# Kernel optimization log

Hardware: AMD Instinct MI355X
Metric: run time of the kernel (lower is better)

## Reference

```python
import jax, jax.numpy as jnp
import numpy as np

N_EXPERTS = 8
TOP_K = 2
HIDDEN = 768
INTER = 2048

def setup_inputs() -> dict:
    key = jax.random.key(0)
    ks = jax.random.split(key, 12)
    s_in = 1.0 / np.sqrt(HIDDEN)
    s_mid = 1.0 / np.sqrt(INTER)
    return {
        "x": jax.random.normal(ks[0], (4, 64, 64, HIDDEN), dtype=jnp.float32),
        # gate: nn.Parameter(randn(E, d))
        "gate_w": jax.random.normal(ks[1], (N_EXPERTS, HIDDEN), dtype=jnp.float32),
        # routed experts, stacked: fc1 (d->f), fc2 (f->d)
        "fc1_w": jax.random.uniform(ks[2], (N_EXPERTS, INTER, HIDDEN), jnp.float32, -s_in, s_in),
        "fc1_b": jax.random.uniform(ks[3], (N_EXPERTS, INTER), jnp.float32, -s_in, s_in),
        "fc2_w": jax.random.uniform(ks[4], (N_EXPERTS, HIDDEN, INTER), jnp.float32, -s_mid, s_mid),
        "fc2_b": jax.random.uniform(ks[5], (N_EXPERTS, HIDDEN), jnp.float32, -s_mid, s_mid),
        # shared MLP (gated): w1 (d->f), w3 (d->f), w2 (f->d)
        "w1_w": jax.random.uniform(ks[6], (INTER, HIDDEN), jnp.float32, -s_in, s_in),
        "w1_b": jax.random.uniform(ks[7], (INTER,), jnp.float32, -s_in, s_in),
        "w3_w": jax.random.uniform(ks[8], (INTER, HIDDEN), jnp.float32, -s_in, s_in),
        "w3_b": jax.random.uniform(ks[9], (INTER,), jnp.float32, -s_in, s_in),
        "w2_w": jax.random.uniform(ks[10], (HIDDEN, INTER), jnp.float32, -s_mid, s_mid),
        "w2_b": jax.random.uniform(ks[11], (HIDDEN,), jnp.float32, -s_mid, s_mid),
    }

def _gelu(h):
    # torch nn.GELU / F.gelu default = exact (erf) form
    return jax.nn.gelu(h, approximate=False)

def reference(x, gate_w, fc1_w, fc1_b, fc2_w, fc2_b,
              w1_w, w1_b, w3_w, w3_b, w2_w, w2_b):
    B, H, W, C = x.shape
    xf = x.reshape(-1, C)                                  # [T, d]
    # gate: softmax over experts, top-k, renormalize
    scores = jax.nn.softmax(xf @ gate_w.T, axis=-1)        # [T, E]
    top_v, top_i = jax.lax.top_k(scores, TOP_K)            # [T, k]
    top_v = top_v / jnp.sum(top_v, axis=-1, keepdims=True)
    # routed experts: dense-mask combine (weight 0 => zero contribution,
    # same math as gather-GEMM-scatter without data-dependent shapes)
    out = jnp.zeros_like(xf)
    for e in range(N_EXPERTS):
        w_e = jnp.sum(jnp.where(top_i == e, top_v, 0.0), axis=-1)   # [T]
        h = _gelu(xf @ fc1_w[e].T + fc1_b[e])                        # [T, f]
        y = h @ fc2_w[e].T + fc2_b[e]                                # [T, d]
        out = out + w_e[:, None] * y
    # shared gated MLP
    shared = (_gelu(xf @ w1_w.T + w1_b) * (xf @ w3_w.T + w3_b)) @ w2_w.T + w2_b
    return (out + shared).reshape(B, H, W, C)
```

## Files before the change

### kernel.cpp

```cpp
#include <hip/hip_runtime.h>
#include <math.h>

#define T_TOK 16384
#define DH 768
#define DF 2048
#define NE 8
#define NSLOT (2 * T_TOK)
#define MT_ROUTED 264
#define NROW_H (MT_ROUTED * 128)

typedef __attribute__((ext_vector_type(8))) short bf16x8;
typedef __attribute__((ext_vector_type(4))) float f32x4;

__device__ __forceinline__ unsigned short f2bf(float f) {
  union { float f; unsigned int u; } v; v.f = f;
  unsigned int u = v.u;
  u += 0x7fffu + ((u >> 16) & 1u);
  return (unsigned short)(u >> 16);
}

__device__ __forceinline__ float gelu_exact(float x) {
  return 0.5f * x * (1.0f + erff(x * 0.70710678118654752440f));
}

__device__ __forceinline__ void async_cp16(void* lds, const void* g) {
  __builtin_amdgcn_global_load_lds(
      (const __attribute__((address_space(1))) unsigned int*)(unsigned long long)g,
      (__attribute__((address_space(3))) unsigned int*)(unsigned int)(unsigned long long)lds,
      16, 0, 0);
}

__global__ __launch_bounds__(256) void conv_f32_bf16(
    const float* __restrict__ src, unsigned short* __restrict__ dst, int n4) {
  int i = blockIdx.x * blockDim.x + threadIdx.x;
  if (i >= n4) return;
  const float4 v = ((const float4*)src)[i];
  union { unsigned short us[4]; unsigned long long u64; } o;
  o.us[0] = f2bf(v.x); o.us[1] = f2bf(v.y); o.us[2] = f2bf(v.z); o.us[3] = f2bf(v.w);
  ((unsigned long long*)dst)[i] = o.u64;
}

__global__ __launch_bounds__(256) void gate_topk(
    const float* __restrict__ x, const float* __restrict__ gw,
    unsigned short* __restrict__ xb, int* __restrict__ eids,
    float* __restrict__ wts) {
  const int wave = threadIdx.x >> 6;
  const int lane = threadIdx.x & 63;
  const int t = blockIdx.x * 4 + wave;
  float4 xv[3];
#pragma unroll
  for (int i = 0; i < 3; ++i) {
    const int c = i * 256 + lane * 4;
    xv[i] = *(const float4*)&x[(long)t * DH + c];
    ushort4 o;
    o.x = f2bf(xv[i].x); o.y = f2bf(xv[i].y);
    o.z = f2bf(xv[i].z); o.w = f2bf(xv[i].w);
    *(ushort4*)&xb[(long)t * DH + c] = o;
  }
  float s[NE];
#pragma unroll
  for (int e = 0; e < NE; ++e) {
    float a = 0.f;
#pragma unroll
    for (int i = 0; i < 3; ++i) {
      const float4 g = *(const float4*)&gw[e * DH + i * 256 + lane * 4];
      a += xv[i].x * g.x + xv[i].y * g.y + xv[i].z * g.z + xv[i].w * g.w;
    }
    s[e] = a;
  }
#pragma unroll
  for (int off = 32; off >= 1; off >>= 1) {
#pragma unroll
    for (int e = 0; e < NE; ++e) s[e] += __shfl_xor(s[e], off);
  }
  if (lane == 0) {
    float b1 = s[0]; int i1 = 0;
#pragma unroll
    for (int e = 1; e < NE; ++e) { if (s[e] > b1) { b1 = s[e]; i1 = e; } }
    float b2 = -3.4e38f; int i2 = 0;
#pragma unroll
    for (int e = 0; e < NE; ++e) {
      if (e != i1 && s[e] > b2) { b2 = s[e]; i2 = e; }
    }
    const float ex = expf(b2 - b1);
    eids[2 * t]     = i1; wts[2 * t]     = 1.f / (1.f + ex);
    eids[2 * t + 1] = i2; wts[2 * t + 1] = ex / (1.f + ex);
  }
}

__global__ __launch_bounds__(256) void hist_k(
    const int* __restrict__ eids, int* __restrict__ hcur) {
  const int j = blockIdx.x * 256 + threadIdx.x;
  const int lane = threadIdx.x & 63;
  const int eid = eids[j];
#pragma unroll
  for (int e = 0; e < NE; ++e) {
    const unsigned long long m = __ballot(eid == e);
    const int tot = __popcll(m);
    if (tot && lane == (__ffsll((long long)m) - 1)) atomicAdd(&hcur[e * 64], tot);
  }
}

__global__ void scan_k(const int* __restrict__ hcur, int* __restrict__ sched,
                       int* __restrict__ cur2) {
  if (threadIdx.x == 0) {
    int b = 0;
#pragma unroll
    for (int e = 0; e < NE; ++e) {
      const int c = hcur[e * 64];
      sched[e] = b; sched[9 + e] = c; cur2[e * 64] = b;
      b += (c + 127) & ~127;
    }
    sched[8] = b;
  }
}

__global__ __launch_bounds__(256) void scatter_k(
    const int* __restrict__ eids, const float* __restrict__ wts,
    int* __restrict__ cur2, int* __restrict__ slot_tok,
    float* __restrict__ slot_wt) {
  const int j = blockIdx.x * 256 + threadIdx.x;
  const int lane = threadIdx.x & 63;
  const int eid = eids[j];
  const float w = wts[j];
#pragma unroll
  for (int e = 0; e < NE; ++e) {
    const unsigned long long m = __ballot(eid == e);
    const int tot = __popcll(m);
    if (!tot) continue;
    const int leader = __ffsll((long long)m) - 1;
    int b = 0;
    if (lane == leader) b = atomicAdd(&cur2[e * 64], tot);
    b = __shfl(b, leader);
    if (eid == e) {
      const int pos = b + __popcll(m & ((1ull << lane) - 1));
      slot_tok[pos] = j;
      slot_wt[pos] = w;
    }
  }
}

template <int MODE>
__global__ __launch_bounds__(256, 2) void gemm_k(
    const unsigned short* __restrict__ A, const unsigned short* __restrict__ B1,
    const unsigned short* __restrict__ B2, const float* __restrict__ bias1,
    const float* __restrict__ bias2, float* __restrict__ outF,
    unsigned short* __restrict__ outH, int K,
    const int* __restrict__ sched, const int* __restrict__ slot_tok,
    const float* __restrict__ slot_wt) {
  const int tid = threadIdx.x;
  const int wave = tid >> 6;
  const int lane = tid & 63;
  const int wm = wave >> 1, wn = wave & 1;
  const int l16 = lane & 15, quad = lane >> 4;
  const int n0 = blockIdx.x * 128;
  const int m0 = blockIdx.y * 128;

  const unsigned short* Bbase = B1;
  const float* bias = bias1;
  int cnt_end = 0;
  if constexpr (MODE == 1 || MODE == 3) {
    if (m0 >= sched[8]) return;
    int e = 0;
#pragma unroll
    for (int i = 1; i < NE; ++i) { if (m0 >= sched[i]) e = i; }
    cnt_end = sched[e] + sched[9 + e];
    Bbase = B1 + (long)e * ((MODE == 1) ? (long)DF * DH : (long)DH * DF);
    bias = bias1 + e * ((MODE == 1) ? DF : DH);
  }

  __shared__ __align__(16) unsigned short As[128 * 32];
  __shared__ __align__(16) unsigned short Bs[128 * 32];
  __shared__ __align__(16) unsigned short Cs[(MODE == 0) ? 128 * 32 : 16];

  const int srow0 = wave * 16 + (lane >> 2);
  const int srow1 = 64 + srow0;
  const int scol = (lane & 3) * 8;

  long ar0, ar1;
  if constexpr (MODE == 1) {
    const int p0 = m0 + srow0, p1 = m0 + srow1;
    const int t0 = (p0 < cnt_end) ? (slot_tok[p0] >> 1) : 0;
    const int t1 = (p1 < cnt_end) ? (slot_tok[p1] >> 1) : 0;
    ar0 = (long)t0 * K; ar1 = (long)t1 * K;
  } else {
    ar0 = (long)(m0 + srow0) * K;
    ar1 = (long)(m0 + srow1) * K;
  }
  const unsigned short* ap0 = A + ar0 + scol;
  const unsigned short* ap1 = A + ar1 + scol;
  const unsigned short* bp0 = Bbase + (long)(n0 + srow0) * K + scol;
  const unsigned short* bp1 = Bbase + (long)(n0 + srow1) * K + scol;
  const unsigned short* cp0 = nullptr; const unsigned short* cp1 = nullptr;
  if constexpr (MODE == 0) {
    cp0 = B2 + (long)(n0 + srow0) * K + scol;
    cp1 = B2 + (long)(n0 + srow1) * K + scol;
  }

  unsigned short* AsW = &As[wave * 512];
  unsigned short* BsW = &Bs[wave * 512];
  unsigned short* CsW = nullptr;
  if constexpr (MODE == 0) CsW = &Cs[wave * 512];

  f32x4 acc[4][4];
  f32x4 acc2[(MODE == 0) ? 4 : 1][(MODE == 0) ? 4 : 1];
#pragma unroll
  for (int i = 0; i < 4; ++i) {
#pragma unroll
    for (int j = 0; j < 4; ++j) {
      acc[i][j] = {0.f, 0.f, 0.f, 0.f};
      if constexpr (MODE == 0) acc2[i][j] = {0.f, 0.f, 0.f, 0.f};
    }
  }

  const int KT = K >> 5;
  for (int kt = 0; kt < KT; ++kt) {
    const int ko = kt << 5;
    async_cp16(AsW,        ap0 + ko);
    async_cp16(AsW + 2048, ap1 + ko);
    async_cp16(BsW,        bp0 + ko);
    async_cp16(BsW + 2048, bp1 + ko);
    if constexpr (MODE == 0) {
      async_cp16(CsW,        cp0 + ko);
      async_cp16(CsW + 2048, cp1 + ko);
    }
    __syncthreads();

    bf16x8 af[4], bfr[4], cfr[(MODE == 0) ? 4 : 1];
#pragma unroll
    for (int mi = 0; mi < 4; ++mi)
      af[mi] = *(const bf16x8*)&As[(wm * 64 + mi * 16 + l16) * 32 + quad * 8];
#pragma unroll
    for (int ni = 0; ni < 4; ++ni) {
      bfr[ni] = *(const bf16x8*)&Bs[(wn * 64 + ni * 16 + l16) * 32 + quad * 8];
      if constexpr (MODE == 0)
        cfr[ni] = *(const bf16x8*)&Cs[(wn * 64 + ni * 16 + l16) * 32 + quad * 8];
    }
#pragma unroll
    for (int mi = 0; mi < 4; ++mi) {
#pragma unroll
      for (int ni = 0; ni < 4; ++ni) {
        acc[mi][ni] = __builtin_amdgcn_mfma_f32_16x16x32_bf16(
            af[mi], bfr[ni], acc[mi][ni], 0, 0, 0);
        if constexpr (MODE == 0)
          acc2[mi][ni] = __builtin_amdgcn_mfma_f32_16x16x32_bf16(
              af[mi], cfr[ni], acc2[mi][ni], 0, 0, 0);
      }
    }
    __syncthreads();
  }

#pragma unroll
  for (int mi = 0; mi < 4; ++mi) {
#pragma unroll
    for (int r = 0; r < 4; ++r) {
      const int row = m0 + wm * 64 + mi * 16 + quad * 4 + r;
      if constexpr (MODE == 3) {
        if (row < cnt_end) {
          const int t = slot_tok[row] >> 1;
          const float w = slot_wt[row];
#pragma unroll
          for (int ni = 0; ni < 4; ++ni) {
            const int c = n0 + wn * 64 + ni * 16 + l16;
            atomicAdd(&outF[(long)t * DH + c], w * (acc[mi][ni][r] + bias[c]));
          }
        }
      } else if constexpr (MODE == 2) {
#pragma unroll
        for (int ni = 0; ni < 4; ++ni) {
          const int c = n0 + wn * 64 + ni * 16 + l16;
          outF[(long)row * DH + c] = acc[mi][ni][r] + bias[c];
        }
      } else if constexpr (MODE == 1) {
#pragma unroll
        for (int ni = 0; ni < 4; ++ni) {
          const int c = n0 + wn * 64 + ni * 16 + l16;
          outH[(long)row * DF + c] = f2bf(gelu_exact(acc[mi][ni][r] + bias[c]));
        }
      } else {
#pragma unroll
        for (int ni = 0; ni < 4; ++ni) {
          const int c = n0 + wn * 64 + ni * 16 + l16;
          const float h1 = acc[mi][ni][r] + bias[c];
          const float h3 = acc2[mi][ni][r] + bias2[c];
          outH[(long)row * DF + c] = f2bf(gelu_exact(h1) * h3);
        }
      }
    }
  }
}

extern "C" void kernel_launch(void* const* d_in, const int* in_sizes, int n_in,
                              void* d_out, int out_size, void* d_ws, size_t ws_size,
                              hipStream_t stream) {
  const float* x     = (const float*)d_in[0];
  const float* gw    = (const float*)d_in[1];
  const float* fc1w  = (const float*)d_in[2];
  const float* fc1bs = (const float*)d_in[3];
  const float* fc2w  = (const float*)d_in[4];
  const float* fc2bs = (const float*)d_in[5];
  const float* w1w   = (const float*)d_in[6];
  const float* w1bs  = (const float*)d_in[7];
  const float* w3w   = (const float*)d_in[8];
  const float* w3bs  = (const float*)d_in[9];
  const float* w2w   = (const float*)d_in[10];
  const float* w2bs  = (const float*)d_in[11];
  float* out = (float*)d_out;

  char* p = (char*)d_ws;
  auto take = [&](size_t b) { char* r = p; p += (b + 255) & ~(size_t)255; return r; };
  unsigned short* xb   = (unsigned short*)take((size_t)T_TOK * DH * 2);
  unsigned short* fc1b = (unsigned short*)take((size_t)NE * DF * DH * 2);
  unsigned short* fc2b = (unsigned short*)take((size_t)NE * DH * DF * 2);
  unsigned short* w1b  = (unsigned short*)take((size_t)DF * DH * 2);
  unsigned short* w3b  = (unsigned short*)take((size_t)DF * DH * 2);
  unsigned short* w2b  = (unsigned short*)take((size_t)DH * DF * 2);
  unsigned short* h    = (unsigned short*)take((size_t)NROW_H * DF * 2);
  int*   eids     = (int*)take((size_t)NSLOT * 4);
  float* wts      = (float*)take((size_t)NSLOT * 4);
  int*   hcur     = (int*)take(NE * 64 * 4);
  int*   cur2     = (int*)take(NE * 64 * 4);
  int*   sched    = (int*)take(32 * 4);
  int*   slot_tok = (int*)take((size_t)NROW_H * 4);
  float* slot_wt  = (float*)take((size_t)NROW_H * 4);

  hipMemsetAsync(hcur, 0, NE * 64 * sizeof(int), stream);

  auto conv = [&](const float* s, unsigned short* d, long n) {
    int n4 = (int)(n >> 2);
    conv_f32_bf16<<<(n4 + 255) / 256, 256, 0, stream>>>(s, d, n4);
  };
  conv(fc1w, fc1b, (long)NE * DF * DH);
  conv(fc2w, fc2b, (long)NE * DH * DF);
  conv(w1w, w1b, (long)DF * DH);
  conv(w3w, w3b, (long)DF * DH);
  conv(w2w, w2b, (long)DH * DF);

  gate_topk<<<T_TOK / 4, 256, 0, stream>>>(x, gw, xb, eids, wts);
  hist_k<<<NSLOT / 256, 256, 0, stream>>>(eids, hcur);
  scan_k<<<1, 64, 0, stream>>>(hcur, sched, cur2);
  scatter_k<<<NSLOT / 256, 256, 0, stream>>>(eids, wts, cur2, slot_tok, slot_wt);

  gemm_k<0><<<dim3(DF / 128, T_TOK / 128), 256, 0, stream>>>(
      xb, w1b, w3b, w1bs, w3bs, nullptr, h, DH, nullptr, nullptr, nullptr);
  gemm_k<2><<<dim3(DH / 128, T_TOK / 128), 256, 0, stream>>>(
      h, w2b, nullptr, w2bs, nullptr, out, nullptr, DF, nullptr, nullptr, nullptr);

  gemm_k<1><<<dim3(DF / 128, MT_ROUTED), 256, 0, stream>>>(
      xb, fc1b, nullptr, fc1bs, nullptr, nullptr, h, DH, sched, slot_tok, slot_wt);
  gemm_k<3><<<dim3(DH / 128, MT_ROUTED), 256, 0, stream>>>(
      h, fc2b, nullptr, fc2bs, nullptr, out, nullptr, DF, sched, slot_tok, slot_wt);
}
```

Baseline: 851.1 us.

## Replace routed atomic scatter with bf16 staging combined in shared-MLP epilogue

The routed fc2 GEMM no longer scatters with float atomicAdd into the output. It writes per-slot results as bf16 rows into a staging buffer that reuses the converted fc1 weight region plus an extra workspace chunk. The shared w2 GEMM epilogue then gathers each token's two slot rows through a new slot_pos map and adds the weighted expert outputs, so every output element is written once. GEMM launches also become 1D grids with an XCD-interleaved block-to-tile mapping. The cost is an extra bf16 round-trip and rounding of the expert outputs, and the old atomic path is kept as a fallback when the workspace is too small.

```diff
diff --git a/kernel.cpp b/kernel.cpp
--- a/kernel.cpp
+++ b/kernel.cpp
@@ -18,9 +18,17 @@
   u += 0x7fffu + ((u >> 16) & 1u);
   return (unsigned short)(u >> 16);
 }
+__device__ __forceinline__ float bf2f(unsigned short s) {
+  union { unsigned int u; float f; } v; v.u = ((unsigned int)s) << 16; return v.f;
+}
 
 __device__ __forceinline__ float gelu_exact(float x) {
   return 0.5f * x * (1.0f + erff(x * 0.70710678118654752440f));
+}
+
+__device__ __forceinline__ unsigned short* yrow(unsigned short* ylo,
+                                                unsigned short* yhi, int s) {
+  return (s < T_TOK) ? (ylo + (long)s * DH) : (yhi + (long)(s - T_TOK) * DH);
 }
 
 __device__ __forceinline__ void async_cp16(void* lds, const void* g) {
@@ -118,7 +126,7 @@
 __global__ __launch_bounds__(256) void scatter_k(
     const int* __restrict__ eids, const float* __restrict__ wts,
     int* __restrict__ cur2, int* __restrict__ slot_tok,
-    float* __restrict__ slot_wt) {
+    float* __restrict__ slot_wt, int* __restrict__ slot_pos) {
   const int j = blockIdx.x * 256 + threadIdx.x;
   const int lane = threadIdx.x & 63;
   const int eid = eids[j];
@@ -136,36 +144,42 @@
       const int pos = b + __popcll(m & ((1ull << lane) - 1));
       slot_tok[pos] = j;
       slot_wt[pos] = w;
-    }
-  }
-}
-
-template <int MODE>
+      slot_pos[j] = pos;
+    }
+  }
+}
+
+template <int MODE, int GX, int GTOT>
 __global__ __launch_bounds__(256, 2) void gemm_k(
     const unsigned short* __restrict__ A, const unsigned short* __restrict__ B1,
     const unsigned short* __restrict__ B2, const float* __restrict__ bias1,
     const float* __restrict__ bias2, float* __restrict__ outF,
     unsigned short* __restrict__ outH, int K,
     const int* __restrict__ sched, const int* __restrict__ slot_tok,
-    const float* __restrict__ slot_wt) {
+    const int* __restrict__ slot_pos, const float* __restrict__ wts,
+    unsigned short* __restrict__ ylo, unsigned short* __restrict__ yhi) {
+  constexpr int BPX = (GTOT + 7) / 8;
+  const int id = blockIdx.x;
+  const int yx = (id & 7) * BPX + (id >> 3);
+  const int n0 = (yx % GX) * 128;
+  const int m0 = (yx / GX) * 128;
+
   const int tid = threadIdx.x;
   const int wave = tid >> 6;
   const int lane = tid & 63;
   const int wm = wave >> 1, wn = wave & 1;
   const int l16 = lane & 15, quad = lane >> 4;
-  const int n0 = blockIdx.x * 128;
-  const int m0 = blockIdx.y * 128;
 
   const unsigned short* Bbase = B1;
   const float* bias = bias1;
   int cnt_end = 0;
-  if constexpr (MODE == 1 || MODE == 3) {
+  if constexpr (MODE == 1 || MODE == 3 || MODE == 4) {
     if (m0 >= sched[8]) return;
     int e = 0;
 #pragma unroll
     for (int i = 1; i < NE; ++i) { if (m0 >= sched[i]) e = i; }
     cnt_end = sched[e] + sched[9 + e];
-    Bbase = B1 + (long)e * ((MODE == 1) ? (long)DF * DH : (long)DH * DF);
+    Bbase = B1 + (long)e * ((long)DF * DH);
     bias = bias1 + e * ((MODE == 1) ? DF : DH);
   }
 
@@ -256,9 +270,16 @@
     for (int r = 0; r < 4; ++r) {
       const int row = m0 + wm * 64 + mi * 16 + quad * 4 + r;
       if constexpr (MODE == 3) {
+        unsigned short* yr = yrow(ylo, yhi, row);
+#pragma unroll
+        for (int ni = 0; ni < 4; ++ni) {
+          const int c = n0 + wn * 64 + ni * 16 + l16;
+          yr[c] = f2bf(acc[mi][ni][r] + bias[c]);
+        }
+      } else if constexpr (MODE == 4) {
         if (row < cnt_end) {
           const int t = slot_tok[row] >> 1;
-          const float w = slot_wt[row];
+          const float w = wts[row];
 #pragma unroll
           for (int ni = 0; ni < 4; ++ni) {
             const int c = n0 + wn * 64 + ni * 16 + l16;
@@ -266,6 +287,17 @@
           }
         }
       } else if constexpr (MODE == 2) {
+        const int s0 = slot_pos[2 * row], s1 = slot_pos[2 * row + 1];
+        const float w0 = wts[2 * row], w1 = wts[2 * row + 1];
+        const unsigned short* y0 = yrow(ylo, yhi, s0);
+        const unsigned short* y1 = yrow(ylo, yhi, s1);
+#pragma unroll
+        for (int ni = 0; ni < 4; ++ni) {
+          const int c = n0 + wn * 64 + ni * 16 + l16;
+          outF[(long)row * DH + c] =
+              acc[mi][ni][r] + bias[c] + w0 * bf2f(y0[c]) + w1 * bf2f(y1[c]);
+        }
+      } else if constexpr (MODE == 5) {
 #pragma unroll
         for (int ni = 0; ni < 4; ++ni) {
           const int c = n0 + wn * 64 + ni * 16 + l16;
@@ -323,6 +355,12 @@
   int*   sched    = (int*)take(32 * 4);
   int*   slot_tok = (int*)take((size_t)NROW_H * 4);
   float* slot_wt  = (float*)take((size_t)NROW_H * 4);
+  int*   slot_pos = (int*)take((size_t)NSLOT * 4);
+
+  const size_t yhi_bytes = (size_t)(NROW_H - T_TOK) * DH * 2;
+  const bool pathA = ((size_t)(p - (char*)d_ws) + yhi_bytes) <= ws_size;
+  unsigned short* ylo = fc1b;
+  unsigned short* yhi = pathA ? (unsigned short*)take(yhi_bytes) : nullptr;
 
   hipMemsetAsync(hcur, 0, NE * 64 * sizeof(int), stream);
 
@@ -339,15 +377,34 @@
   gate_topk<<<T_TOK / 4, 256, 0, stream>>>(x, gw, xb, eids, wts);
   hist_k<<<NSLOT / 256, 256, 0, stream>>>(eids, hcur);
   scan_k<<<1, 64, 0, stream>>>(hcur, sched, cur2);
-  scatter_k<<<NSLOT / 256, 256, 0, stream>>>(eids, wts, cur2, slot_tok, slot_wt);
-
-  gemm_k<0><<<dim3(DF / 128, T_TOK / 128), 256, 0, stream>>>(
-      xb, w1b, w3b, w1bs, w3bs, nullptr, h, DH, nullptr, nullptr, nullptr);
-  gemm_k<2><<<dim3(DH / 128, T_TOK / 128), 256, 0, stream>>>(
-      h, w2b, nullptr, w2bs, nullptr, out, nullptr, DF, nullptr, nullptr, nullptr);
-
-  gemm_k<1><<<dim3(DF / 128, MT_ROUTED), 256, 0, stream>>>(
-      xb, fc1b, nullptr, fc1bs, nullptr, nullptr, h, DH, sched, slot_tok, slot_wt);
-  gemm_k<3><<<dim3(DH / 128, MT_ROUTED), 256, 0, stream>>>(
-      h, fc2b, nullptr, fc2bs, nullptr, out, nullptr, DF, sched, slot_tok, slot_wt);
-}
+  scatter_k<<<NSLOT / 256, 256, 0, stream>>>(eids, wts, cur2, slot_tok, slot_wt,
+                                             slot_pos);
+
+  if (pathA) {
+    gemm_k<1, 16, 16 * MT_ROUTED><<<16 * MT_ROUTED, 256, 0, stream>>>(
+        xb, fc1b, nullptr, fc1bs, nullptr, nullptr, h, DH,
+        sched, slot_tok, nullptr, nullptr, nullptr, nullptr);
+    gemm_k<3, 6, 6 * MT_ROUTED><<<6 * MT_ROUTED, 256, 0, stream>>>(
+        h, fc2b, nullptr, fc2bs, nullptr, nullptr, nullptr, DF,
+        sched, nullptr, nullptr, nullptr, ylo, yhi);
+    gemm_k<0, 16, 16 * (T_TOK / 128)><<<16 * (T_TOK / 128), 256, 0, stream>>>(
+        xb, w1b, w3b, w1bs, w3bs, nullptr, h, DH,
+        nullptr, nullptr, nullptr, nullptr, nullptr, nullptr);
+    gemm_k<2, 6, 6 * (T_TOK / 128)><<<6 * (T_TOK / 128), 256, 0, stream>>>(
+        h, w2b, nullptr, w2bs, nullptr, out, nullptr, DF,
+        nullptr, nullptr, slot_pos, wts, ylo, yhi);
+  } else {
+    gemm_k<0, 16, 16 * (T_TOK / 128)><<<16 * (T_TOK / 128), 256, 0, stream>>>(
+        xb, w1b, w3b, w1bs, w3bs, nullptr, h, DH,
+        nullptr, nullptr, nullptr, nullptr, nullptr, nullptr);
+    gemm_k<5, 6, 6 * (T_TOK / 128)><<<6 * (T_TOK / 128), 256, 0, stream>>>(
+        h, w2b, nullptr, w2bs, nullptr, out, nullptr, DF,
+        nullptr, nullptr, nullptr, nullptr, nullptr, nullptr);
+    gemm_k<1, 16, 16 * MT_ROUTED><<<16 * MT_ROUTED, 256, 0, stream>>>(
+        xb, fc1b, nullptr, fc1bs, nullptr, nullptr, h, DH,
+        sched, slot_tok, nullptr, nullptr, nullptr, nullptr);
+    gemm_k<4, 6, 6 * MT_ROUTED><<<6 * MT_ROUTED, 256, 0, stream>>>(
+        h, fc2b, nullptr, fc2bs, nullptr, out, nullptr, DF,
+        sched, slot_tok, nullptr, slot_wt, nullptr, nullptr);
+  }
+}
```

New measurement: 774.5 us. 9.0% less time.
